# Kernel tuning notes

Measured on AMD Instinct MI355X. Metric: run time of the kernel, lower is better.

Reference implementation:

```python
import jax, jax.numpy as jnp
import numpy as np

VOCAB, E = 100000, 128
B, W = 1024, 5
MARGIN = 0.1


def setup_inputs() -> dict:
    key = jax.random.key(0)
    k1, k2, k3, k4, k5 = jax.random.split(key, 5)
    mu = jax.random.uniform(k1, (VOCAB, E), dtype=jnp.float32) * 0.1  # uniform(0, mu_0)
    sigma = 0.5 + 1.5 * jax.random.uniform(k2, (VOCAB, E), dtype=jnp.float32)  # uniform(sigma_min, sigma_max)
    target = jax.random.randint(k3, (B, 1), 0, VOCAB)
    context_pos = jax.random.randint(k4, (B, W), 0, VOCAB)
    context_neg = jax.random.randint(k5, (B, W), 0, VOCAB)
    return {"mu": mu, "sigma": sigma, "target": target,
            "context_pos": context_pos, "context_neg": context_neg}


def _diag_kl(m1, s1, m2, s2):
    # KL( N(m1, diag(s1)) || N(m2, diag(s2)) ); s are variances (cov = sigma * I in torch code)
    # 0.5 * [ tr(S2^-1 S1) + (m2-m1)^T S2^-1 (m2-m1) - E + log|S2| - log|S1| ]
    d = m2 - m1
    return 0.5 * jnp.sum(s1 / s2 + d * d / s2 - 1.0 + jnp.log(s2) - jnp.log(s1), axis=-1)


def reference(mu, sigma, target, context_pos, context_neg):
    m_t, s_t = mu[target], sigma[target]            # [B,1,E]
    m_p, s_p = mu[context_pos], sigma[context_pos]  # [B,W,E]
    m_n, s_n = mu[context_neg], sigma[context_neg]  # [B,W,E]
    kl_pos = _diag_kl(m_t, s_t, m_p, s_p)           # [B,W]
    kl_neg = _diag_kl(m_t, s_t, m_n, s_n)           # [B,W]
    loss = jnp.maximum(0.0, MARGIN - kl_pos + kl_neg).sum(axis=1).mean()
    return loss
```

## Files before the change

### kernel.cpp

```cpp
#include <hip/hip_runtime.h>


constexpr int E = 128;
constexpr int W = 5;
constexpr int NB = 1024;
constexpr float MARGIN = 0.1f;
constexpr float LN2 = 0.69314718055994530942f;

__global__ __launch_bounds__(64) void gauss_emb_kl(
    const float* __restrict__ mu, const float* __restrict__ sigma,
    const int* __restrict__ target, const int* __restrict__ cpos,
    const int* __restrict__ cneg, float* __restrict__ partial)
{
    const int b = blockIdx.x;
    const int lane = threadIdx.x;

    const int t = target[b];
    const float2 m1 = ((const float2*)(mu    + (size_t)t * E))[lane];
    const float2 s1 = ((const float2*)(sigma + (size_t)t * E))[lane];

    int idx[2 * W];
#pragma unroll
    for (int k = 0; k < W; ++k) idx[k]     = cpos[b * W + k];
#pragma unroll
    for (int k = 0; k < W; ++k) idx[W + k] = cneg[b * W + k];

    float2 m2[2 * W], s2[2 * W];
#pragma unroll
    for (int k = 0; k < 2 * W; ++k) {
        m2[k] = ((const float2*)(mu    + (size_t)idx[k] * E))[lane];
        s2[k] = ((const float2*)(sigma + (size_t)idx[k] * E))[lane];
    }

    const float l1x = __log2f(s1.x);
    const float l1y = __log2f(s1.y);

    float kl[2 * W];
#pragma unroll
    for (int k = 0; k < 2 * W; ++k) {
        const float dx = m2[k].x - m1.x;
        const float dy = m2[k].y - m1.y;
        const float cx = (s1.x + dx * dx) / s2[k].x + LN2 * (__log2f(s2[k].x) - l1x);
        const float cy = (s1.y + dy * dy) / s2[k].y + LN2 * (__log2f(s2[k].y) - l1y);
        kl[k] = cx + cy - 2.0f;
    }

#pragma unroll
    for (int k = 0; k < 2 * W; ++k) {
#pragma unroll
        for (int off = 32; off >= 1; off >>= 1)
            kl[k] += __shfl_xor(kl[k], off, 64);
    }

    if (lane == 0) {
        float h = 0.f;
#pragma unroll
        for (int w = 0; w < W; ++w)
            h += fmaxf(0.f, MARGIN - 0.5f * kl[w] + 0.5f * kl[W + w]);
        partial[b] = h;
    }
}

__global__ __launch_bounds__(256) void gauss_emb_reduce(
    const float* __restrict__ partial, float* __restrict__ out)
{
    __shared__ float wave_sums[4];
    float s = 0.f;
    for (int i = threadIdx.x; i < NB; i += 256) s += partial[i];
#pragma unroll
    for (int off = 32; off >= 1; off >>= 1)
        s += __shfl_xor(s, off, 64);
    const int wid = threadIdx.x >> 6;
    if ((threadIdx.x & 63) == 0) wave_sums[wid] = s;
    __syncthreads();
    if (threadIdx.x == 0) {
        const float tot = wave_sums[0] + wave_sums[1] + wave_sums[2] + wave_sums[3];
        out[0] = tot * (1.0f / (float)NB);
    }
}

extern "C" void kernel_launch(void* const* d_in, const int* in_sizes, int n_in,
                              void* d_out, int out_size, void* d_ws, size_t ws_size,
                              hipStream_t stream)
{
    const float* mu     = (const float*)d_in[0];
    const float* sigma  = (const float*)d_in[1];
    const int*   target = (const int*)d_in[2];
    const int*   cpos   = (const int*)d_in[3];
    const int*   cneg   = (const int*)d_in[4];
    float* partial = (float*)d_ws;

    gauss_emb_kl<<<NB, 64, 0, stream>>>(mu, sigma, target, cpos, cneg, partial);
    gauss_emb_reduce<<<1, 256, 0, stream>>>(partial, (float*)d_out);
}
```

Baseline: 12.20 us.

## Fuse KL and reduction kernels via cooperative launch with grid sync

Merges the per-row KL kernel and the final reduction into one cooperative kernel. A grid-wide barrier replaces the second launch, and block 0 then does the reduction. Blocks now hold four waves (256 threads, 256 blocks) instead of one wave each. This removes one kernel launch and its gap, but adds grid-sync cost and the overhead of a cooperative launch.

New measurement: 43.05 us. 3.53x slower.

```diff
diff --git a/kernel.cpp b/kernel.cpp
--- a/kernel.cpp
+++ b/kernel.cpp
@@ -1,4 +1,7 @@
 #include <hip/hip_runtime.h>
+#include <hip/hip_cooperative_groups.h>
+
+namespace cg = cooperative_groups;
 
 
 constexpr int E = 128;
@@ -7,75 +10,78 @@
 constexpr float MARGIN = 0.1f;
 constexpr float LN2 = 0.69314718055994530942f;
 
-__global__ __launch_bounds__(64) void gauss_emb_kl(
+__global__ __launch_bounds__(256) void gauss_emb_fused(
     const float* __restrict__ mu, const float* __restrict__ sigma,
     const int* __restrict__ target, const int* __restrict__ cpos,
-    const int* __restrict__ cneg, float* __restrict__ partial)
+    const int* __restrict__ cneg, float* __restrict__ partial,
+    float* __restrict__ out)
 {
-    const int b = blockIdx.x;
-    const int lane = threadIdx.x;
+    const int wave = threadIdx.x >> 6;
+    const int lane = threadIdx.x & 63;
+    const int b = blockIdx.x * 4 + wave;
 
-    const int t = target[b];
-    const float2 m1 = ((const float2*)(mu    + (size_t)t * E))[lane];
-    const float2 s1 = ((const float2*)(sigma + (size_t)t * E))[lane];
+    {
+        const int t = target[b];
+        const float2 m1 = ((const float2*)(mu    + (size_t)t * E))[lane];
+        const float2 s1 = ((const float2*)(sigma + (size_t)t * E))[lane];
 
-    int idx[2 * W];
+        int idx[2 * W];
 #pragma unroll
-    for (int k = 0; k < W; ++k) idx[k]     = cpos[b * W + k];
+        for (int k = 0; k < W; ++k) idx[k]     = cpos[b * W + k];
 #pragma unroll
-    for (int k = 0; k < W; ++k) idx[W + k] = cneg[b * W + k];
+        for (int k = 0; k < W; ++k) idx[W + k] = cneg[b * W + k];
 
-    float2 m2[2 * W], s2[2 * W];
+        float2 m2[2 * W], s2[2 * W];
 #pragma unroll
-    for (int k = 0; k < 2 * W; ++k) {
-        m2[k] = ((const float2*)(mu    + (size_t)idx[k] * E))[lane];
-        s2[k] = ((const float2*)(sigma + (size_t)idx[k] * E))[lane];
+        for (int k = 0; k < 2 * W; ++k) {
+            m2[k] = ((const float2*)(mu    + (size_t)idx[k] * E))[lane];
+            s2[k] = ((const float2*)(sigma + (size_t)idx[k] * E))[lane];
+        }
+
+        const float l1x = __log2f(s1.x);
+        const float l1y = __log2f(s1.y);
+
+        float kl[2 * W];
+#pragma unroll
+        for (int k = 0; k < 2 * W; ++k) {
+            const float dx = m2[k].x - m1.x;
+            const float dy = m2[k].y - m1.y;
+            const float cx = (s1.x + dx * dx) / s2[k].x + LN2 * (__log2f(s2[k].x) - l1x);
+            const float cy = (s1.y + dy * dy) / s2[k].y + LN2 * (__log2f(s2[k].y) - l1y);
+            kl[k] = cx + cy - 2.0f;
+        }
+
+#pragma unroll
+        for (int k = 0; k < 2 * W; ++k) {
+#pragma unroll
+            for (int off = 32; off >= 1; off >>= 1)
+                kl[k] += __shfl_xor(kl[k], off, 64);
+        }
+
+        if (lane == 0) {
+            float h = 0.f;
+#pragma unroll
+            for (int w = 0; w < W; ++w)
+                h += fmaxf(0.f, MARGIN - 0.5f * kl[w] + 0.5f * kl[W + w]);
+            partial[b] = h;
+        }
     }
 
-    const float l1x = __log2f(s1.x);
-    const float l1y = __log2f(s1.y);
+    cg::this_grid().sync();
 
-    float kl[2 * W];
-#pragma unroll
-    for (int k = 0; k < 2 * W; ++k) {
-        const float dx = m2[k].x - m1.x;
-        const float dy = m2[k].y - m1.y;
-        const float cx = (s1.x + dx * dx) / s2[k].x + LN2 * (__log2f(s2[k].x) - l1x);
-        const float cy = (s1.y + dy * dy) / s2[k].y + LN2 * (__log2f(s2[k].y) - l1y);
-        kl[k] = cx + cy - 2.0f;
-    }
-
-#pragma unroll
-    for (int k = 0; k < 2 * W; ++k) {
+    if (blockIdx.x == 0) {
+        const int t = threadIdx.x;
+        float s = partial[t] + partial[t + 256] + partial[t + 512] + partial[t + 768];
 #pragma unroll
         for (int off = 32; off >= 1; off >>= 1)
-            kl[k] += __shfl_xor(kl[k], off, 64);
-    }
-
-    if (lane == 0) {
-        float h = 0.f;
-#pragma unroll
-        for (int w = 0; w < W; ++w)
-            h += fmaxf(0.f, MARGIN - 0.5f * kl[w] + 0.5f * kl[W + w]);
-        partial[b] = h;
-    }
-}
-
-__global__ __launch_bounds__(256) void gauss_emb_reduce(
-    const float* __restrict__ partial, float* __restrict__ out)
-{
-    __shared__ float wave_sums[4];
-    float s = 0.f;
-    for (int i = threadIdx.x; i < NB; i += 256) s += partial[i];
-#pragma unroll
-    for (int off = 32; off >= 1; off >>= 1)
-        s += __shfl_xor(s, off, 64);
-    const int wid = threadIdx.x >> 6;
-    if ((threadIdx.x & 63) == 0) wave_sums[wid] = s;
-    __syncthreads();
-    if (threadIdx.x == 0) {
-        const float tot = wave_sums[0] + wave_sums[1] + wave_sums[2] + wave_sums[3];
-        out[0] = tot * (1.0f / (float)NB);
+            s += __shfl_xor(s, off, 64);
+        __shared__ float wave_sums[4];
+        if ((t & 63) == 0) wave_sums[t >> 6] = s;
+        __syncthreads();
+        if (t == 0) {
+            const float tot = wave_sums[0] + wave_sums[1] + wave_sums[2] + wave_sums[3];
+            out[0] = tot * (1.0f / (float)NB);
+        }
     }
 }
 
@@ -89,7 +95,10 @@
     const int*   cpos   = (const int*)d_in[3];
     const int*   cneg   = (const int*)d_in[4];
     float* partial = (float*)d_ws;
+    float* out     = (float*)d_out;
 
-    gauss_emb_kl<<<NB, 64, 0, stream>>>(mu, sigma, target, cpos, cneg, partial);
-    gauss_emb_reduce<<<1, 256, 0, stream>>>(partial, (float*)d_out);
+    void* args[] = { (void*)&mu, (void*)&sigma, (void*)&target,
+                     (void*)&cpos, (void*)&cneg, (void*)&partial, (void*)&out };
+    hipLaunchCooperativeKernel((const void*)gauss_emb_fused,
+                               dim3(NB / 4), dim3(256), args, 0, stream);
 }
```

## Split wave into pos/neg halves, fold KL difference algebraically, use rcp

Applied to the files above, without the earlier changes.

The wave is split into two 32-lane halves, one for positive and one for negative contexts, each loading float4 chunks. The target-only terms (log s1 and the constant) cancel in kl_neg - kl_pos, so each lane computes a signed partial and a single shuffle reduction yields the difference per window. This halves the shuffle reductions and the log work on the target. Division is replaced by the hardware reciprocal approximation, which may cost some precision. The final reduce is reduced to one wave reading float4 values with no shared memory or barrier.

Result: faster. 11.38 us (-6.7%).

```diff
diff --git a/kernel.cpp b/kernel.cpp
--- a/kernel.cpp
+++ b/kernel.cpp
@@ -12,71 +12,80 @@
     const int* __restrict__ target, const int* __restrict__ cpos,
     const int* __restrict__ cneg, float* __restrict__ partial)
 {
-    const int b = blockIdx.x;
+    const int b    = blockIdx.x;
     const int lane = threadIdx.x;
+    const int half = lane >> 5;
+    const int sub  = lane & 31;
 
     const int t = target[b];
-    const float2 m1 = ((const float2*)(mu    + (size_t)t * E))[lane];
-    const float2 s1 = ((const float2*)(sigma + (size_t)t * E))[lane];
+    const float4 m1 = ((const float4*)(mu    + (size_t)t * E))[sub];
+    const float4 s1 = ((const float4*)(sigma + (size_t)t * E))[sub];
 
-    int idx[2 * W];
+    int idx[W];
 #pragma unroll
-    for (int k = 0; k < W; ++k) idx[k]     = cpos[b * W + k];
-#pragma unroll
-    for (int k = 0; k < W; ++k) idx[W + k] = cneg[b * W + k];
-
-    float2 m2[2 * W], s2[2 * W];
-#pragma unroll
-    for (int k = 0; k < 2 * W; ++k) {
-        m2[k] = ((const float2*)(mu    + (size_t)idx[k] * E))[lane];
-        s2[k] = ((const float2*)(sigma + (size_t)idx[k] * E))[lane];
+    for (int w = 0; w < W; ++w) {
+        const int ip = cpos[b * W + w];
+        const int in = cneg[b * W + w];
+        idx[w] = half ? in : ip;
     }
 
-    const float l1x = __log2f(s1.x);
-    const float l1y = __log2f(s1.y);
+    float4 m2[W], s2[W];
+#pragma unroll
+    for (int w = 0; w < W; ++w) {
+        m2[w] = ((const float4*)(mu    + (size_t)idx[w] * E))[sub];
+        s2[w] = ((const float4*)(sigma + (size_t)idx[w] * E))[sub];
+    }
 
-    float kl[2 * W];
+    const float sign = half ? 1.0f : -1.0f;
+
+    float dW[W];
 #pragma unroll
-    for (int k = 0; k < 2 * W; ++k) {
-        const float dx = m2[k].x - m1.x;
-        const float dy = m2[k].y - m1.y;
-        const float cx = (s1.x + dx * dx) / s2[k].x + LN2 * (__log2f(s2[k].x) - l1x);
-        const float cy = (s1.y + dy * dy) / s2[k].y + LN2 * (__log2f(s2[k].y) - l1y);
-        kl[k] = cx + cy - 2.0f;
+    for (int w = 0; w < W; ++w) {
+        float acc = 0.f;
+#pragma unroll
+        for (int j = 0; j < 4; ++j) {
+            const float m1j = ((const float*)&m1)[j];
+            const float s1j = ((const float*)&s1)[j];
+            const float m2j = ((const float*)&m2[w])[j];
+            const float s2j = ((const float*)&s2[w])[j];
+            const float d   = m2j - m1j;
+            acc += (s1j + d * d) * __builtin_amdgcn_rcpf(s2j)
+                 + LN2 * __log2f(s2j);
+        }
+        dW[w] = sign * acc;
     }
 
 #pragma unroll
-    for (int k = 0; k < 2 * W; ++k) {
+    for (int w = 0; w < W; ++w) {
 #pragma unroll
         for (int off = 32; off >= 1; off >>= 1)
-            kl[k] += __shfl_xor(kl[k], off, 64);
+            dW[w] += __shfl_xor(dW[w], off, 64);
     }
 
     if (lane == 0) {
         float h = 0.f;
 #pragma unroll
         for (int w = 0; w < W; ++w)
-            h += fmaxf(0.f, MARGIN - 0.5f * kl[w] + 0.5f * kl[W + w]);
+            h += fmaxf(0.f, MARGIN + 0.5f * dW[w]);
         partial[b] = h;
     }
 }
 
-__global__ __launch_bounds__(256) void gauss_emb_reduce(
+__global__ __launch_bounds__(64) void gauss_emb_reduce(
     const float* __restrict__ partial, float* __restrict__ out)
 {
-    __shared__ float wave_sums[4];
+    const int lane = threadIdx.x;
+    const float4* p4 = (const float4*)partial;
     float s = 0.f;
-    for (int i = threadIdx.x; i < NB; i += 256) s += partial[i];
+#pragma unroll
+    for (int k = 0; k < 4; ++k) {
+        const float4 v = p4[lane + 64 * k];
+        s += v.x + v.y + v.z + v.w;
+    }
 #pragma unroll
     for (int off = 32; off >= 1; off >>= 1)
         s += __shfl_xor(s, off, 64);
-    const int wid = threadIdx.x >> 6;
-    if ((threadIdx.x & 63) == 0) wave_sums[wid] = s;
-    __syncthreads();
-    if (threadIdx.x == 0) {
-        const float tot = wave_sums[0] + wave_sums[1] + wave_sums[2] + wave_sums[3];
-        out[0] = tot * (1.0f / (float)NB);
-    }
+    if (lane == 0) out[0] = s * (1.0f / (float)NB);
 }
 
 extern "C" void kernel_launch(void* const* d_in, const int* in_sizes, int n_in,
@@ -91,5 +100,5 @@
     float* partial = (float*)d_ws;
 
     gauss_emb_kl<<<NB, 64, 0, stream>>>(mu, sigma, target, cpos, cneg, partial);
-    gauss_emb_reduce<<<1, 256, 0, stream>>>(partial, (float*)d_out);
+    gauss_emb_reduce<<<1, 64, 0, stream>>>(partial, (float*)d_out);
 }
```
